# Performance work log

Measured on AMD Instinct MI355X. Metric: run time of the kernel, lower is better.

The kernel has to match this reference:

```python
import jax, jax.numpy as jnp
import numpy as np

B, N, D, K = 8, 8192, 256, 3


def setup_inputs() -> dict:
    key = jax.random.key(0)
    k0, k1, k2, k3 = jax.random.split(key, 4)
    basic_units = jax.random.normal(k0, (B, N, D), dtype=jnp.float32)
    # learned params: offset/modulation linear weights (K, D) and conv weight (D, D, K)
    offset_w = jax.random.normal(k1, (K, D), dtype=jnp.float32) * 0.02
    mod_w = jax.random.normal(k2, (K, D), dtype=jnp.float32) * 0.1
    fan_in = D * K
    weight = jax.random.normal(k3, (D, D, K), dtype=jnp.float32) * np.sqrt(2.0 / fan_in)
    return {"basic_units": basic_units, "offset_w": offset_w, "mod_w": mod_w, "weight": weight}


def reference(basic_units, offset_w, mod_w, weight):
    b, n, d = basic_units.shape
    k = weight.shape[2]
    # offsets and modulation per token per kernel tap: (B, N, K)
    offset = jnp.einsum('bnd,kd->bnk', basic_units, offset_w)
    modulation = jax.nn.sigmoid(jnp.einsum('bnd,kd->bnk', basic_units, mod_w))
    # base sampling position i + k - K//2, perturbed by data-dependent offset
    base = (jnp.arange(n)[:, None] + jnp.arange(k)[None, :] - k // 2).astype(basic_units.dtype)  # (N, K)
    pos = base[None, :, :] + offset  # (B, N, K)
    valid = (pos >= 0) & (pos < n)
    floor_f = jnp.clip(jnp.floor(pos), 0, n - 1)
    fi = floor_f.astype(jnp.int32)               # (B, N, K)
    ci = jnp.minimum(fi + 1, n - 1)
    w_ceil = pos - floor_f
    w_floor = 1.0 - w_ceil

    def gather(idx):
        # x[b, idx[b, i, k], :] -> (B, N, K, D)
        return jnp.take_along_axis(basic_units, idx.reshape(b, n * k, 1), axis=1).reshape(b, n, k, d)

    interp = w_floor[..., None] * gather(fi) + w_ceil[..., None] * gather(ci)  # (B, N, K, D)
    # modulate, zero out-of-range taps, then per-tap matmul summed over taps
    modulated = interp * (modulation * valid.astype(interp.dtype))[..., None]
    out = jnp.einsum('dek,bike->bid', weight, modulated)
    return out
```

## Files before the change

kernel.cpp:

```cpp
#include <hip/hip_runtime.h>
#include <hip/hip_bf16.h>
#include <cstdint>


#define N_TOK 8192
#define DIM   256
#define KW    768
#define BM    128
#define BN    128
#define BK    32

typedef unsigned short u16;
typedef __attribute__((ext_vector_type(4))) float    floatx4;
typedef __attribute__((ext_vector_type(8))) __bf16   bf16x8;
typedef __attribute__((ext_vector_type(8))) u16      ushortx8;

__device__ __forceinline__ u16 f32_to_bf16_rne(float f) {
    uint32_t u = __float_as_uint(f);
    u += 0x7fffu + ((u >> 16) & 1u);
    return (u16)(u >> 16);
}

__global__ __launch_bounds__(256) void coef_kernel(
    const float* __restrict__ x, const float* __restrict__ offw,
    const float* __restrict__ modw, int4* __restrict__ coef)
{
    const int wave = threadIdx.x >> 6;
    const int lane = threadIdx.x & 63;
    const int t = blockIdx.x * 4 + wave;

    const float4 xv = ((const float4*)(x + (size_t)t * DIM))[lane];
    float s[6];
#pragma unroll
    for (int k = 0; k < 3; ++k) {
        float4 wv = ((const float4*)(offw + k * DIM))[lane];
        s[k]     = xv.x * wv.x + xv.y * wv.y + xv.z * wv.z + xv.w * wv.w;
        float4 mv = ((const float4*)(modw + k * DIM))[lane];
        s[3 + k] = xv.x * mv.x + xv.y * mv.y + xv.z * mv.z + xv.w * mv.w;
    }
#pragma unroll
    for (int d = 1; d < 64; d <<= 1) {
#pragma unroll
        for (int i = 0; i < 6; ++i) s[i] += __shfl_xor(s[i], d, 64);
    }
    if (lane < 3) {
        const int k = lane;
        const int n = t & (N_TOK - 1);
        float pos   = (float)(n + k - 1) + s[k];
        bool  valid = (pos >= 0.0f) && (pos < (float)N_TOK);
        float ff = floorf(pos);
        ff = fminf(fmaxf(ff, 0.0f), (float)(N_TOK - 1));
        int   fi = (int)ff;
        int   ci = min(fi + 1, N_TOK - 1);
        float wc = pos - ff;
        float m  = valid ? (1.0f / (1.0f + expf(-s[3 + k]))) : 0.0f;
        coef[t * 3 + k] = make_int4(fi, ci,
                                    __float_as_int((1.0f - wc) * m),
                                    __float_as_int(wc * m));
    }
}

__global__ __launch_bounds__(256) void packw_kernel(
    const float* __restrict__ W, u16* __restrict__ WB)
{
    const int d = blockIdx.x;
    const int e = threadIdx.x;
#pragma unroll
    for (int k = 0; k < 3; ++k)
        WB[d * KW + k * DIM + e] = f32_to_bf16_rne(W[d * KW + e * 3 + k]);
}

__global__ __launch_bounds__(256) void deform_gemm_kernel(
    const float* __restrict__ x, const u16* __restrict__ WB,
    const int4* __restrict__ coef, float* __restrict__ out)
{
    __shared__ __align__(16) u16 As[2][BM * 40];
    __shared__ __align__(16) u16 Bs[2][BN * 40];

    const int tid  = threadIdx.x;
    const int wave = tid >> 6;
    const int lane = tid & 63;
    const int mtile = blockIdx.x >> 1;
    const int ntile = blockIdx.x & 1;
    const int t0 = mtile * BM;
    const int n0 = ntile * BN;
    const float* xb = x + (size_t)(t0 / N_TOK) * N_TOK * DIM;

    const int tl = tid >> 1;
    const int eh = tid & 1;
    const int wm = (wave & 1) * 64;
    const int wn = (wave >> 1) * 64;
    const int lrow = lane & 15;
    const int lq   = lane >> 4;

    const int4 cc0 = coef[(size_t)(t0 + tl) * 3 + 0];
    const int4 cc1 = coef[(size_t)(t0 + tl) * 3 + 1];
    const int4 cc2 = coef[(size_t)(t0 + tl) * 3 + 2];

    float4 pf[4], pc[4];
    uint4  pb0, pb1;
    float  wA, wC;

    auto loadg = [&](int kk) {
        const int tap = kk >> 3;
        const int4 c = (tap == 0) ? cc0 : (tap == 1 ? cc1 : cc2);
        const int e0 = (kk & 7) * 32 + eh * 16;
        wA = __int_as_float(c.z);
        wC = __int_as_float(c.w);
        const float4* rowf = (const float4*)(xb + (size_t)c.x * DIM + e0);
        const float4* rowc = (const float4*)(xb + (size_t)c.y * DIM + e0);
#pragma unroll
        for (int j = 0; j < 4; ++j) { pf[j] = rowf[j]; pc[j] = rowc[j]; }
        const uint4* g = (const uint4*)(WB + (size_t)(n0 + tl) * KW + kk * BK + eh * 16);
        pb0 = g[0];
        pb1 = g[1];
    };

    auto packstore = [&](int buf) {
        uint32_t p[8];
#pragma unroll
        for (int j = 0; j < 4; ++j) {
            float r0 = wA * pf[j].x + wC * pc[j].x;
            float r1 = wA * pf[j].y + wC * pc[j].y;
            float r2 = wA * pf[j].z + wC * pc[j].z;
            float r3 = wA * pf[j].w + wC * pc[j].w;
            p[j * 2 + 0] = __builtin_amdgcn_perm(__float_as_uint(r1), __float_as_uint(r0), 0x07060302u);
            p[j * 2 + 1] = __builtin_amdgcn_perm(__float_as_uint(r3), __float_as_uint(r2), 0x07060302u);
        }
        uint4* adst = (uint4*)&As[buf][tl * 40 + eh * 16];
        adst[0] = make_uint4(p[0], p[1], p[2], p[3]);
        adst[1] = make_uint4(p[4], p[5], p[6], p[7]);
        uint4* bdst = (uint4*)&Bs[buf][tl * 40 + eh * 16];
        bdst[0] = pb0;
        bdst[1] = pb1;
    };

    loadg(0);
    packstore(0);
    loadg(1);

    floatx4 acc[4][4];
#pragma unroll
    for (int i = 0; i < 4; ++i)
#pragma unroll
        for (int j = 0; j < 4; ++j) acc[i][j] = (floatx4){0.f, 0.f, 0.f, 0.f};

    __syncthreads();

    for (int kk = 0; kk < 24; ++kk) {
        const int cur = kk & 1;
        bf16x8 af[4], bfv[4];
#pragma unroll
        for (int i = 0; i < 4; ++i)
            af[i] = __builtin_bit_cast(bf16x8, *(const ushortx8*)&As[cur][(wm + i * 16 + lrow) * 40 + lq * 8]);
#pragma unroll
        for (int j = 0; j < 4; ++j)
            bfv[j] = __builtin_bit_cast(bf16x8, *(const ushortx8*)&Bs[cur][(wn + j * 16 + lrow) * 40 + lq * 8]);
        if (kk < 23) packstore(cur ^ 1);
        if (kk < 22) loadg(kk + 2);
#pragma unroll
        for (int i = 0; i < 4; ++i)
#pragma unroll
            for (int j = 0; j < 4; ++j)
                acc[i][j] = __builtin_amdgcn_mfma_f32_16x16x32_bf16(af[i], bfv[j], acc[i][j], 0, 0, 0);
        __syncthreads();
    }

#pragma unroll
    for (int i = 0; i < 4; ++i) {
#pragma unroll
        for (int r = 0; r < 4; ++r) {
            const int token = t0 + wm + i * 16 + lq * 4 + r;
            float* op = out + (size_t)token * DIM + n0 + wn + lrow;
#pragma unroll
            for (int j = 0; j < 4; ++j) op[j * 16] = acc[i][j][r];
        }
    }
}

extern "C" void kernel_launch(void* const* d_in, const int* in_sizes, int n_in,
                              void* d_out, int out_size, void* d_ws, size_t ws_size,
                              hipStream_t stream)
{
    const float* x    = (const float*)d_in[0];
    const float* offw = (const float*)d_in[1];
    const float* modw = (const float*)d_in[2];
    const float* W    = (const float*)d_in[3];
    float* out = (float*)d_out;

    const int tot_tok = 8 * N_TOK;
    int4* coef = (int4*)d_ws;
    u16*  WB   = (u16*)((char*)d_ws + (size_t)tot_tok * 3 * 16);

    coef_kernel<<<tot_tok / 4, 256, 0, stream>>>(x, offw, modw, coef);
    packw_kernel<<<DIM, 256, 0, stream>>>(W, WB);
    deform_gemm_kernel<<<(tot_tok / BM) * (DIM / BN), 256, 0, stream>>>(x, WB, coef, out);
}
```

Before: 191.9 us.

## Fuse coefficient computation into GEMM and widen tile to full output width

```diff
diff --git a/kernel.cpp b/kernel.cpp
--- a/kernel.cpp
+++ b/kernel.cpp
@@ -7,7 +7,7 @@
 #define DIM   256
 #define KW    768
 #define BM    128
-#define BN    128
+#define BN    256
 #define BK    32
 
 typedef unsigned short u16;
@@ -21,45 +21,6 @@
     return (u16)(u >> 16);
 }
 
-__global__ __launch_bounds__(256) void coef_kernel(
-    const float* __restrict__ x, const float* __restrict__ offw,
-    const float* __restrict__ modw, int4* __restrict__ coef)
-{
-    const int wave = threadIdx.x >> 6;
-    const int lane = threadIdx.x & 63;
-    const int t = blockIdx.x * 4 + wave;
-
-    const float4 xv = ((const float4*)(x + (size_t)t * DIM))[lane];
-    float s[6];
-#pragma unroll
-    for (int k = 0; k < 3; ++k) {
-        float4 wv = ((const float4*)(offw + k * DIM))[lane];
-        s[k]     = xv.x * wv.x + xv.y * wv.y + xv.z * wv.z + xv.w * wv.w;
-        float4 mv = ((const float4*)(modw + k * DIM))[lane];
-        s[3 + k] = xv.x * mv.x + xv.y * mv.y + xv.z * mv.z + xv.w * mv.w;
-    }
-#pragma unroll
-    for (int d = 1; d < 64; d <<= 1) {
-#pragma unroll
-        for (int i = 0; i < 6; ++i) s[i] += __shfl_xor(s[i], d, 64);
-    }
-    if (lane < 3) {
-        const int k = lane;
-        const int n = t & (N_TOK - 1);
-        float pos   = (float)(n + k - 1) + s[k];
-        bool  valid = (pos >= 0.0f) && (pos < (float)N_TOK);
-        float ff = floorf(pos);
-        ff = fminf(fmaxf(ff, 0.0f), (float)(N_TOK - 1));
-        int   fi = (int)ff;
-        int   ci = min(fi + 1, N_TOK - 1);
-        float wc = pos - ff;
-        float m  = valid ? (1.0f / (1.0f + expf(-s[3 + k]))) : 0.0f;
-        coef[t * 3 + k] = make_int4(fi, ci,
-                                    __float_as_int((1.0f - wc) * m),
-                                    __float_as_int(wc * m));
-    }
-}
-
 __global__ __launch_bounds__(256) void packw_kernel(
     const float* __restrict__ W, u16* __restrict__ WB)
 {
@@ -70,9 +31,10 @@
         WB[d * KW + k * DIM + e] = f32_to_bf16_rne(W[d * KW + e * 3 + k]);
 }
 
-__global__ __launch_bounds__(256) void deform_gemm_kernel(
-    const float* __restrict__ x, const u16* __restrict__ WB,
-    const int4* __restrict__ coef, float* __restrict__ out)
+__global__ __launch_bounds__(512, 4) void deform_gemm_kernel(
+    const float* __restrict__ x, const float* __restrict__ offw,
+    const float* __restrict__ modw, const u16* __restrict__ WB,
+    float* __restrict__ out)
 {
     __shared__ __align__(16) u16 As[2][BM * 40];
     __shared__ __align__(16) u16 Bs[2][BN * 40];
@@ -80,46 +42,80 @@
     const int tid  = threadIdx.x;
     const int wave = tid >> 6;
     const int lane = tid & 63;
-    const int mtile = blockIdx.x >> 1;
-    const int ntile = blockIdx.x & 1;
-    const int t0 = mtile * BM;
-    const int n0 = ntile * BN;
+    const int t0 = blockIdx.x * BM;
     const float* xb = x + (size_t)(t0 / N_TOK) * N_TOK * DIM;
 
-    const int tl = tid >> 1;
-    const int eh = tid & 1;
+    const int tq  = tid >> 2;
+    const int qd  = tid & 3;
+    const int brow = tid >> 1;
+    const int bh   = tid & 1;
     const int wm = (wave & 1) * 64;
     const int wn = (wave >> 1) * 64;
     const int lrow = lane & 15;
     const int lq   = lane >> 4;
 
-    const int4 cc0 = coef[(size_t)(t0 + tl) * 3 + 0];
-    const int4 cc1 = coef[(size_t)(t0 + tl) * 3 + 1];
-    const int4 cc2 = coef[(size_t)(t0 + tl) * 3 + 2];
+    int4 cc0, cc1, cc2;
+    {
+        const int t_abs = t0 + tq;
+        const float4* xr = (const float4*)(x + (size_t)t_abs * DIM + qd * 64);
+        float s[6] = {0.f, 0.f, 0.f, 0.f, 0.f, 0.f};
+#pragma unroll
+        for (int j = 0; j < 16; ++j) {
+            const float4 xv = xr[j];
+#pragma unroll
+            for (int k = 0; k < 3; ++k) {
+                const float4 wv = ((const float4*)(offw + k * DIM + qd * 64))[j];
+                s[k]     += xv.x * wv.x + xv.y * wv.y + xv.z * wv.z + xv.w * wv.w;
+                const float4 mv = ((const float4*)(modw + k * DIM + qd * 64))[j];
+                s[3 + k] += xv.x * mv.x + xv.y * mv.y + xv.z * mv.z + xv.w * mv.w;
+            }
+        }
+#pragma unroll
+        for (int i = 0; i < 6; ++i) {
+            s[i] += __shfl_xor(s[i], 1, 64);
+            s[i] += __shfl_xor(s[i], 2, 64);
+        }
+        const int n = t_abs & (N_TOK - 1);
+        int4 cc[3];
+#pragma unroll
+        for (int k = 0; k < 3; ++k) {
+            float pos   = (float)(n + k - 1) + s[k];
+            bool  valid = (pos >= 0.0f) && (pos < (float)N_TOK);
+            float ff = floorf(pos);
+            ff = fminf(fmaxf(ff, 0.0f), (float)(N_TOK - 1));
+            int   fi = (int)ff;
+            int   ci = min(fi + 1, N_TOK - 1);
+            float wc = pos - ff;
+            float m  = valid ? (1.0f / (1.0f + expf(-s[3 + k]))) : 0.0f;
+            cc[k] = make_int4(fi, ci, __float_as_int((1.0f - wc) * m),
+                                      __float_as_int(wc * m));
+        }
+        cc0 = cc[0]; cc1 = cc[1]; cc2 = cc[2];
+    }
 
-    float4 pf[4], pc[4];
+    float4 pf[2], pc[2];
     uint4  pb0, pb1;
     float  wA, wC;
 
     auto loadg = [&](int kk) {
         const int tap = kk >> 3;
         const int4 c = (tap == 0) ? cc0 : (tap == 1 ? cc1 : cc2);
-        const int e0 = (kk & 7) * 32 + eh * 16;
+        const int e0 = (kk & 7) * 32 + qd * 8;
         wA = __int_as_float(c.z);
         wC = __int_as_float(c.w);
         const float4* rowf = (const float4*)(xb + (size_t)c.x * DIM + e0);
         const float4* rowc = (const float4*)(xb + (size_t)c.y * DIM + e0);
-#pragma unroll
-        for (int j = 0; j < 4; ++j) { pf[j] = rowf[j]; pc[j] = rowc[j]; }
-        const uint4* g = (const uint4*)(WB + (size_t)(n0 + tl) * KW + kk * BK + eh * 16);
+        pf[0] = rowf[0]; pf[1] = rowf[1];
+        pc[0] = rowc[0]; pc[1] = rowc[1];
+        const uint4* g = (const uint4*)(WB + (size_t)brow * KW + kk * BK + bh * 16);
         pb0 = g[0];
         pb1 = g[1];
     };
 
     auto packstore = [&](int buf) {
-        uint32_t p[8];
+        uint32_t p[4];
 #pragma unroll
-        for (int j = 0; j < 4; ++j) {
+        for (int j = 0; j < 2; ++j) {
             float r0 = wA * pf[j].x + wC * pc[j].x;
             float r1 = wA * pf[j].y + wC * pc[j].y;
             float r2 = wA * pf[j].z + wC * pc[j].z;
@@ -127,10 +123,8 @@
             p[j * 2 + 0] = __builtin_amdgcn_perm(__float_as_uint(r1), __float_as_uint(r0), 0x07060302u);
             p[j * 2 + 1] = __builtin_amdgcn_perm(__float_as_uint(r3), __float_as_uint(r2), 0x07060302u);
         }
-        uint4* adst = (uint4*)&As[buf][tl * 40 + eh * 16];
-        adst[0] = make_uint4(p[0], p[1], p[2], p[3]);
-        adst[1] = make_uint4(p[4], p[5], p[6], p[7]);
-        uint4* bdst = (uint4*)&Bs[buf][tl * 40 + eh * 16];
+        *(uint4*)&As[buf][tq * 40 + qd * 8] = make_uint4(p[0], p[1], p[2], p[3]);
+        uint4* bdst = (uint4*)&Bs[buf][brow * 40 + bh * 16];
         bdst[0] = pb0;
         bdst[1] = pb1;
     };
@@ -171,7 +165,7 @@
 #pragma unroll
         for (int r = 0; r < 4; ++r) {
             const int token = t0 + wm + i * 16 + lq * 4 + r;
-            float* op = out + (size_t)token * DIM + n0 + wn + lrow;
+            float* op = out + (size_t)token * DIM + wn + lrow;
 #pragma unroll
             for (int j = 0; j < 4; ++j) op[j * 16] = acc[i][j][r];
         }
@@ -188,11 +182,9 @@
     const float* W    = (const float*)d_in[3];
     float* out = (float*)d_out;
 
+    u16* WB = (u16*)d_ws;
+
+    packw_kernel<<<DIM, 256, 0, stream>>>(W, WB);
     const int tot_tok = 8 * N_TOK;
-    int4* coef = (int4*)d_ws;
-    u16*  WB   = (u16*)((char*)d_ws + (size_t)tot_tok * 3 * 16);
-
-    coef_kernel<<<tot_tok / 4, 256, 0, stream>>>(x, offw, modw, coef);
-    packw_kernel<<<DIM, 256, 0, stream>>>(W, WB);
-    deform_gemm_kernel<<<(tot_tok / BM) * (DIM / BN), 256, 0, stream>>>(x, WB, coef, out);
+    deform_gemm_kernel<<<tot_tok / BM, 512, 0, stream>>>(x, offw, modw, WB, out);
 }
```

Result: slower. 250.3 us (+30.4%).

## Load weight fragments straight from global into registers and swizzle block order

Applied to the files above, without the earlier changes.

```diff
diff --git a/kernel.cpp b/kernel.cpp
--- a/kernel.cpp
+++ b/kernel.cpp
@@ -75,13 +75,14 @@
     const int4* __restrict__ coef, float* __restrict__ out)
 {
     __shared__ __align__(16) u16 As[2][BM * 40];
-    __shared__ __align__(16) u16 Bs[2][BN * 40];
 
     const int tid  = threadIdx.x;
     const int wave = tid >> 6;
     const int lane = tid & 63;
-    const int mtile = blockIdx.x >> 1;
-    const int ntile = blockIdx.x & 1;
+
+    const int g  = blockIdx.x;
+    const int mtile = (g >> 4) * 8 + (g & 7);
+    const int ntile = (g >> 3) & 1;
     const int t0 = mtile * BM;
     const int n0 = ntile * BN;
     const float* xb = x + (size_t)(t0 / N_TOK) * N_TOK * DIM;
@@ -98,10 +99,9 @@
     const int4 cc2 = coef[(size_t)(t0 + tl) * 3 + 2];
 
     float4 pf[4], pc[4];
-    uint4  pb0, pb1;
     float  wA, wC;
 
-    auto loadg = [&](int kk) {
+    auto loadA = [&](int kk) {
         const int tap = kk >> 3;
         const int4 c = (tap == 0) ? cc0 : (tap == 1 ? cc1 : cc2);
         const int e0 = (kk & 7) * 32 + eh * 16;
@@ -111,12 +111,9 @@
         const float4* rowc = (const float4*)(xb + (size_t)c.y * DIM + e0);
 #pragma unroll
         for (int j = 0; j < 4; ++j) { pf[j] = rowf[j]; pc[j] = rowc[j]; }
-        const uint4* g = (const uint4*)(WB + (size_t)(n0 + tl) * KW + kk * BK + eh * 16);
-        pb0 = g[0];
-        pb1 = g[1];
     };
 
-    auto packstore = [&](int buf) {
+    auto packstoreA = [&](int buf) {
         uint32_t p[8];
 #pragma unroll
         for (int j = 0; j < 4; ++j) {
@@ -130,14 +127,19 @@
         uint4* adst = (uint4*)&As[buf][tl * 40 + eh * 16];
         adst[0] = make_uint4(p[0], p[1], p[2], p[3]);
         adst[1] = make_uint4(p[4], p[5], p[6], p[7]);
-        uint4* bdst = (uint4*)&Bs[buf][tl * 40 + eh * 16];
-        bdst[0] = pb0;
-        bdst[1] = pb1;
     };
 
-    loadg(0);
-    packstore(0);
-    loadg(1);
+    uint4 bq[4];
+    auto loadB = [&](int kk) {
+#pragma unroll
+        for (int j = 0; j < 4; ++j)
+            bq[j] = *(const uint4*)(WB + (size_t)(n0 + wn + j * 16 + lrow) * KW + kk * BK + lq * 8);
+    };
+
+    loadA(0);
+    packstoreA(0);
+    loadA(1);
+    loadB(0);
 
     floatx4 acc[4][4];
 #pragma unroll
@@ -149,20 +151,22 @@
 
     for (int kk = 0; kk < 24; ++kk) {
         const int cur = kk & 1;
-        bf16x8 af[4], bfv[4];
+        bf16x8 af[4];
 #pragma unroll
         for (int i = 0; i < 4; ++i)
             af[i] = __builtin_bit_cast(bf16x8, *(const ushortx8*)&As[cur][(wm + i * 16 + lrow) * 40 + lq * 8]);
-#pragma unroll
-        for (int j = 0; j < 4; ++j)
-            bfv[j] = __builtin_bit_cast(bf16x8, *(const ushortx8*)&Bs[cur][(wn + j * 16 + lrow) * 40 + lq * 8]);
-        if (kk < 23) packstore(cur ^ 1);
-        if (kk < 22) loadg(kk + 2);
+        uint4 bc[4];
+#pragma unroll
+        for (int j = 0; j < 4; ++j) bc[j] = bq[j];
+        if (kk < 23) loadB(kk + 1);
+        if (kk < 23) packstoreA(cur ^ 1);
+        if (kk < 22) loadA(kk + 2);
 #pragma unroll
         for (int i = 0; i < 4; ++i)
 #pragma unroll
             for (int j = 0; j < 4; ++j)
-                acc[i][j] = __builtin_amdgcn_mfma_f32_16x16x32_bf16(af[i], bfv[j], acc[i][j], 0, 0, 0);
+                acc[i][j] = __builtin_amdgcn_mfma_f32_16x16x32_bf16(
+                    af[i], __builtin_bit_cast(bf16x8, bc[j]), acc[i][j], 0, 0, 0);
         __syncthreads();
     }
 
@@ -194,5 +198,5 @@
 
     coef_kernel<<<tot_tok / 4, 256, 0, stream>>>(x, offw, modw, coef);
     packw_kernel<<<DIM, 256, 0, stream>>>(W, WB);
-    deform_gemm_kernel<<<(tot_tok / BM) * (DIM / BN), 256, 0, stream>>>(x, WB, coef, out);
-}
+    deform_gemm_kernel<<<(tot_tok / BM) * 2, 256, 0, stream>>>(x, WB, coef, out);
+}
```

Result: slower. 211.1 us (+10.0%).
